# Kernel tuning notes

Measured on AMD Instinct MI355X. Metric: run time of the kernel, lower is better.

The kernel has to match this reference:

```python
import jax, jax.numpy as jnp
import numpy as np

B, T, E, D = 8, 2048, 1024, 64  # batch, seq_len, n_emb, head_dim

def setup_inputs() -> dict:
    key = jax.random.key(0)
    ks = jax.random.split(key, 4)
    scale = 1.0 / np.sqrt(E)
    return {
        "x": jax.random.normal(ks[0], (B, T, E), dtype=jnp.float32),
        "Wq": jax.random.normal(ks[1], (E, D), dtype=jnp.float32) * scale,
        "bq": jnp.zeros((D,), dtype=jnp.float32),
        "Wk": jax.random.normal(ks[2], (E, D), dtype=jnp.float32) * scale,
        "bk": jnp.zeros((D,), dtype=jnp.float32),
        "Wv": jax.random.normal(ks[3], (E, D), dtype=jnp.float32) * scale,
        "bv": jnp.zeros((D,), dtype=jnp.float32),
    }

def reference(x, Wq, bq, Wk, bk, Wv, bv):
    # QKV projections: [B,T,E] @ [E,D] -> [B,T,D]
    q = x @ Wq + bq
    k = x @ Wk + bk
    v = x @ Wv + bv
    d = q.shape[-1]
    # scaled dot-product scores [B,T,T]
    wei = jnp.einsum('btd,bsd->bts', q, k) * (d ** -0.5)
    # causal mask: position t attends to s <= t
    t = wei.shape[1]
    causal = jnp.tril(jnp.ones((t, t), dtype=bool))
    wei = jnp.where(causal, wei, -jnp.inf)
    wei = jax.nn.softmax(wei, axis=-1)
    # attention output [B,T,D]
    return jnp.einsum('bts,bsd->btd', wei, v)
```

## Files before the change

### kernel.cpp

```cpp
#include <hip/hip_runtime.h>
#include <math.h>


#define B_   8
#define T_   2048
#define E_   1024
#define D_   64
#define BT_  (B_ * T_)

typedef __attribute__((ext_vector_type(8))) short s16x8;
typedef __attribute__((ext_vector_type(4))) short s16x4;
typedef __attribute__((ext_vector_type(4))) float f32x4;

__device__ __forceinline__ short f2bf(float f) {
    union { float f; unsigned u; } a; a.f = f;
    unsigned r = a.u + 0x7fffu + ((a.u >> 16) & 1u);
    return (short)(r >> 16);
}

#define MFMA16(a, b, c) __builtin_amdgcn_mfma_f32_16x16x32_bf16((a), (b), (c), 0, 0, 0)

#define DPPF(x, ctrl) __builtin_bit_cast(float, \
    __builtin_amdgcn_update_dpp(0, __builtin_bit_cast(int, (x)), (ctrl), 0xF, 0xF, true))

__device__ __forceinline__ float rsum16(float x) {
    x += DPPF(x, 0xB1);
    x += DPPF(x, 0x4E);
    x += DPPF(x, 0x124);
    x += DPPF(x, 0x128);
    return x;
}

__global__ __launch_bounds__(256) void wtrans_kernel(
    const float* __restrict__ Wq, const float* __restrict__ Wk,
    const float* __restrict__ Wv, short* __restrict__ Wt)
{
    __shared__ float sT[64][65];
    const int sel = blockIdx.x >> 4;
    const int k0  = (blockIdx.x & 15) * 64;
    const float* W = sel == 0 ? Wq : (sel == 1 ? Wk : Wv);
    const int t  = threadIdx.x;
    const int kr = t >> 4, c4 = (t & 15) * 4;
    #pragma unroll
    for (int i = 0; i < 4; ++i) {
        float4 v = *(const float4*)&W[(size_t)(k0 + kr + i * 16) * D_ + c4];
        sT[kr + i * 16][c4 + 0] = v.x; sT[kr + i * 16][c4 + 1] = v.y;
        sT[kr + i * 16][c4 + 2] = v.z; sT[kr + i * 16][c4 + 3] = v.w;
    }
    __syncthreads();
    #pragma unroll
    for (int i = 0; i < 4; ++i) {
        int n  = (t >> 4) + i * 16;
        int kk = (t & 15) * 4;
        s16x4 o;
        o.x = f2bf(sT[kk + 0][n]); o.y = f2bf(sT[kk + 1][n]);
        o.z = f2bf(sT[kk + 2][n]); o.w = f2bf(sT[kk + 3][n]);
        *(s16x4*)&Wt[(size_t)(sel * 64 + n) * E_ + k0 + kk] = o;
    }
}

__global__ __launch_bounds__(256) void qkv_kernel(
    const float* __restrict__ x, const short* __restrict__ Wt,
    const float* __restrict__ bq, const float* __restrict__ bk,
    const float* __restrict__ bv,
    short* __restrict__ Qg, short* __restrict__ Kg, short* __restrict__ VTg)
{
    __shared__ short sX[2][32 * 76];
    const int tid  = threadIdx.x;
    const int lane = tid & 63;
    const int w    = tid >> 6;
    const int l15  = lane & 15, quad = lane >> 4;
    const int t0   = blockIdx.x * 32;
    const int bb   = t0 >> 11;

    const int srow = tid >> 3;
    const int skc  = (tid & 7) * 8;
    const float* px = &x[(size_t)(t0 + srow) * E_ + skc];

    f32x4 acc[3][2];
    #pragma unroll
    for (int a = 0; a < 3; ++a)
        #pragma unroll
        for (int h = 0; h < 2; ++h)
            acc[a][h] = (f32x4){0.f, 0.f, 0.f, 0.f};

    float4 ld0 = *(const float4*)px;
    float4 ld1 = *(const float4*)(px + 4);

    int buf = 0;
    for (int k0 = 0; k0 < E_; k0 += 64) {
        s16x8 pk;
        pk[0] = f2bf(ld0.x); pk[1] = f2bf(ld0.y); pk[2] = f2bf(ld0.z); pk[3] = f2bf(ld0.w);
        pk[4] = f2bf(ld1.x); pk[5] = f2bf(ld1.y); pk[6] = f2bf(ld1.z); pk[7] = f2bf(ld1.w);
        *(s16x8*)&sX[buf][srow * 76 + skc] = pk;
        __syncthreads();

        if (k0 + 64 < E_) {
            const float* p2 = px + k0 + 64;
            ld0 = *(const float4*)p2;
            ld1 = *(const float4*)(p2 + 4);
        }

        s16x8 aw[3][2];
        #pragma unroll
        for (int t3 = 0; t3 < 3; ++t3) {
            const short* pw = &Wt[(size_t)((w * 3 + t3) * 16 + l15) * E_ + k0 + quad * 8];
            aw[t3][0] = *(const s16x8*)pw;
            aw[t3][1] = *(const s16x8*)(pw + 32);
        }
        s16x8 bxf[2][2];
        #pragma unroll
        for (int h = 0; h < 2; ++h) {
            bxf[h][0] = *(const s16x8*)&sX[buf][(h * 16 + l15) * 76 + quad * 8];
            bxf[h][1] = *(const s16x8*)&sX[buf][(h * 16 + l15) * 76 + 32 + quad * 8];
        }
        #pragma unroll
        for (int t3 = 0; t3 < 3; ++t3)
            #pragma unroll
            for (int h = 0; h < 2; ++h) {
                acc[t3][h] = MFMA16(aw[t3][0], bxf[h][0], acc[t3][h]);
                acc[t3][h] = MFMA16(aw[t3][1], bxf[h][1], acc[t3][h]);
            }
        buf ^= 1;
    }

    __syncthreads();
    short* sVT = &sX[0][0];

    #pragma unroll
    for (int t3 = 0; t3 < 3; ++t3) {
        const int nt = w * 3 + t3;
        const int fb = (nt & 3) * 16 + quad * 4;
        const float* bias = nt < 4 ? bq : (nt < 8 ? bk : bv);
        f32x4 bsv = *(const f32x4*)&bias[fb];
        #pragma unroll
        for (int h = 0; h < 2; ++h) {
            const int tok = t0 + h * 16 + l15;
            f32x4 v = acc[t3][h] + bsv;
            if (nt < 4) {
                v *= 0.125f;
                s16x4 o = { f2bf(v[0]), f2bf(v[1]), f2bf(v[2]), f2bf(v[3]) };
                *(s16x4*)&Qg[(size_t)tok * D_ + fb] = o;
            } else if (nt < 8) {
                s16x4 o = { f2bf(v[0]), f2bf(v[1]), f2bf(v[2]), f2bf(v[3]) };
                *(s16x4*)&Kg[(size_t)tok * D_ + fb] = o;
            } else {
                const int lt = h * 16 + l15;
                #pragma unroll
                for (int r = 0; r < 4; ++r)
                    sVT[(fb + r) * 48 + lt] = f2bf(v[r]);
            }
        }
    }
    __syncthreads();
    {
        const int d  = tid >> 2;
        const int tq = (tid & 3) * 8;
        s16x8 vv = *(const s16x8*)&sVT[d * 48 + tq];
        *(s16x8*)&VTg[(size_t)(bb * D_ + d) * T_ + (t0 & (T_ - 1)) + tq] = vv;
    }
}

__global__ __launch_bounds__(256) void attn_kernel(
    const short* __restrict__ Qg, const short* __restrict__ Kg,
    const short* __restrict__ VTg, float* __restrict__ out)
{
    __shared__ char smem[20736];
    short* sP = (short*)smem;
    float* sO = (float*)smem;
    float* sl = (float*)(smem + 20480);

    const int tid  = threadIdx.x;
    const int lane = tid & 63;
    const int w    = tid >> 6;
    const int l15  = lane & 15, quad = lane >> 4;
    const int b    = blockIdx.x & 7;
    const int j    = 127 - (blockIdx.x >> 3);
    const int tq0  = j * 16;
    const int nch  = (j >> 2) + 1;
    const int seg  = (nch + 3) >> 2;
    const int c0   = w * seg;
    const int c1   = (c0 + seg < nch) ? c0 + seg : nch;

    const size_t qoff = ((size_t)b * T_ + tq0 + l15) * D_ + quad * 8;
    const s16x8 aq0 = *(const s16x8*)&Qg[qoff];
    const s16x8 aq1 = *(const s16x8*)&Qg[qoff + 32];

    f32x4 oacc[4];
    float lpart[4] = {0.f, 0.f, 0.f, 0.f};
    #pragma unroll
    for (int nt = 0; nt < 4; ++nt) oacc[nt] = (f32x4){0.f, 0.f, 0.f, 0.f};

    const short* kb = Kg  + (size_t)b * T_ * D_;
    const short* vb = VTg + (size_t)b * D_ * T_;
    short* sPw = sP + w * (16 * 72);

    for (int c = c0; c < c1; ++c) {
        const int s0 = c * 64;

        s16x8 bk[4][2];
        #pragma unroll
        for (int nt = 0; nt < 4; ++nt) {
            const short* pk = kb + (size_t)(s0 + nt * 16 + l15) * D_ + quad * 8;
            bk[nt][0] = *(const s16x8*)pk;
            bk[nt][1] = *(const s16x8*)(pk + 32);
        }
        const f32x4 zz = (f32x4){0.f, 0.f, 0.f, 0.f};
        f32x4 sacc[4];
        #pragma unroll
        for (int nt = 0; nt < 4; ++nt) {
            sacc[nt] = MFMA16(aq0, bk[nt][0], zz);
            sacc[nt] = MFMA16(aq1, bk[nt][1], sacc[nt]);
        }

        s16x8 bv[4][2];
        #pragma unroll
        for (int nt = 0; nt < 4; ++nt) {
            const short* pv = vb + (size_t)(nt * 16 + l15) * T_ + s0 + quad * 8;
            bv[nt][0] = *(const s16x8*)pv;
            bv[nt][1] = *(const s16x8*)(pv + 32);
        }

        const bool diag = (c == nch - 1);
        float p[4][4];
        #pragma unroll
        for (int nt = 0; nt < 4; ++nt)
            #pragma unroll
            for (int r = 0; r < 4; ++r) {
                float e = __expf(sacc[nt][r]);
                if (diag && (s0 + nt * 16 + l15 > tq0 + quad * 4 + r)) e = 0.f;
                p[nt][r] = e;
            }
        #pragma unroll
        for (int r = 0; r < 4; ++r)
            lpart[r] += (p[0][r] + p[1][r]) + (p[2][r] + p[3][r]);

        #pragma unroll
        for (int nt = 0; nt < 4; ++nt)
            #pragma unroll
            for (int r = 0; r < 4; ++r)
                sPw[(quad * 4 + r) * 72 + nt * 16 + l15] = f2bf(p[nt][r]);
        s16x8 ap0 = *(const s16x8*)&sPw[l15 * 72 + quad * 8];
        s16x8 ap1 = *(const s16x8*)&sPw[l15 * 72 + 32 + quad * 8];

        #pragma unroll
        for (int nt = 0; nt < 4; ++nt) {
            oacc[nt] = MFMA16(ap0, bv[nt][0], oacc[nt]);
            oacc[nt] = MFMA16(ap1, bv[nt][1], oacc[nt]);
        }
    }

    f32x4 lv;
    #pragma unroll
    for (int r = 0; r < 4; ++r) lv[r] = rsum16(lpart[r]);

    __syncthreads();
    float* sOw = sO + w * (64 * 20);
    #pragma unroll
    for (int nt = 0; nt < 4; ++nt)
        *(f32x4*)&sOw[(nt * 16 + l15) * 20 + quad * 4] = oacc[nt];
    if (l15 == 0)
        *(f32x4*)&sl[w * 16 + quad * 4] = lv;
    __syncthreads();

    const int d  = tid & 63;
    const int rb = (tid >> 6) * 4;
    f32x4 osum = (f32x4){0.f, 0.f, 0.f, 0.f};
    f32x4 lsum = (f32x4){0.f, 0.f, 0.f, 0.f};
    #pragma unroll
    for (int w2 = 0; w2 < 4; ++w2) {
        osum += *(const f32x4*)&sO[w2 * (64 * 20) + d * 20 + rb];
        lsum += *(const f32x4*)&sl[w2 * 16 + rb];
    }
    #pragma unroll
    for (int i = 0; i < 4; ++i)
        out[((size_t)b * T_ + tq0 + rb + i) * D_ + d] = osum[i] / lsum[i];
}

extern "C" void kernel_launch(void* const* d_in, const int* in_sizes, int n_in,
                              void* d_out, int out_size, void* d_ws, size_t ws_size,
                              hipStream_t stream) {
    (void)in_sizes; (void)n_in; (void)out_size; (void)ws_size;
    const float* x  = (const float*)d_in[0];
    const float* Wq = (const float*)d_in[1];
    const float* bq = (const float*)d_in[2];
    const float* Wk = (const float*)d_in[3];
    const float* bk = (const float*)d_in[4];
    const float* Wv = (const float*)d_in[5];
    const float* bv = (const float*)d_in[6];

    char* ws = (char*)d_ws;
    short* Qg  = (short*)(ws);
    short* Kg  = (short*)(ws + (size_t)2 * 1024 * 1024);
    short* VTg = (short*)(ws + (size_t)4 * 1024 * 1024);
    short* Wt  = (short*)(ws + (size_t)6 * 1024 * 1024);

    wtrans_kernel<<<48, 256, 0, stream>>>(Wq, Wk, Wv, Wt);
    qkv_kernel<<<BT_ / 32, 256, 0, stream>>>(x, Wt, bq, bk, bv, Qg, Kg, VTg);
    attn_kernel<<<B_ * 128, 256, 0, stream>>>(Qg, Kg, VTg, (float*)d_out);
}
```

Measured before the change: 167.8 us.

## Pair short and long causal query tiles per block; deepen x prefetch

The attention kernel now gives each block two 16-row query tiles, j and 127-j. Their combined key chunks are split evenly across the four waves, which balances the triangular causal work and halves the grid to 512 blocks. The QKV projection kernel also prefetches x two k-steps ahead instead of one, to hide more global-load latency. In exchange each attention block does two reductions through shared memory, needs more registers, and has fewer blocks to fill the GPU.

```diff
diff --git a/kernel.cpp b/kernel.cpp
--- a/kernel.cpp
+++ b/kernel.cpp
@@ -84,21 +84,26 @@
         for (int h = 0; h < 2; ++h)
             acc[a][h] = (f32x4){0.f, 0.f, 0.f, 0.f};
 
-    float4 ld0 = *(const float4*)px;
-    float4 ld1 = *(const float4*)(px + 4);
+    float4 lda0 = *(const float4*)px;
+    float4 lda1 = *(const float4*)(px + 4);
+    float4 ldb0 = *(const float4*)(px + 64);
+    float4 ldb1 = *(const float4*)(px + 68);
 
     int buf = 0;
     for (int k0 = 0; k0 < E_; k0 += 64) {
         s16x8 pk;
-        pk[0] = f2bf(ld0.x); pk[1] = f2bf(ld0.y); pk[2] = f2bf(ld0.z); pk[3] = f2bf(ld0.w);
-        pk[4] = f2bf(ld1.x); pk[5] = f2bf(ld1.y); pk[6] = f2bf(ld1.z); pk[7] = f2bf(ld1.w);
+        pk[0] = f2bf(lda0.x); pk[1] = f2bf(lda0.y);
+        pk[2] = f2bf(lda0.z); pk[3] = f2bf(lda0.w);
+        pk[4] = f2bf(lda1.x); pk[5] = f2bf(lda1.y);
+        pk[6] = f2bf(lda1.z); pk[7] = f2bf(lda1.w);
         *(s16x8*)&sX[buf][srow * 76 + skc] = pk;
         __syncthreads();
 
-        if (k0 + 64 < E_) {
-            const float* p2 = px + k0 + 64;
-            ld0 = *(const float4*)p2;
-            ld1 = *(const float4*)(p2 + 4);
+        lda0 = ldb0; lda1 = ldb1;
+        if (k0 + 128 < E_) {
+            const float* p2 = px + k0 + 128;
+            ldb0 = *(const float4*)p2;
+            ldb1 = *(const float4*)(p2 + 4);
         }
 
         s16x8 aw[3][2];
@@ -175,29 +180,37 @@
     const int w    = tid >> 6;
     const int l15  = lane & 15, quad = lane >> 4;
     const int b    = blockIdx.x & 7;
-    const int j    = 127 - (blockIdx.x >> 3);
-    const int tq0  = j * 16;
-    const int nch  = (j >> 2) + 1;
-    const int seg  = (nch + 3) >> 2;
+    const int pr   = blockIdx.x >> 3;
+    const int jA   = pr, jB = 127 - pr;
+    const int tqA  = jA * 16, tqB = jB * 16;
+    const int nchA = (jA >> 2) + 1, nchB = (jB >> 2) + 1;
+    const int tot  = nchA + nchB;
+    const int seg  = (tot + 3) >> 2;
     const int c0   = w * seg;
-    const int c1   = (c0 + seg < nch) ? c0 + seg : nch;
-
-    const size_t qoff = ((size_t)b * T_ + tq0 + l15) * D_ + quad * 8;
-    const s16x8 aq0 = *(const s16x8*)&Qg[qoff];
-    const s16x8 aq1 = *(const s16x8*)&Qg[qoff + 32];
-
-    f32x4 oacc[4];
-    float lpart[4] = {0.f, 0.f, 0.f, 0.f};
-    #pragma unroll
-    for (int nt = 0; nt < 4; ++nt) oacc[nt] = (f32x4){0.f, 0.f, 0.f, 0.f};
+    const int c1   = (c0 + seg < tot) ? c0 + seg : tot;
+
+    const size_t qoffA = ((size_t)b * T_ + tqA + l15) * D_ + quad * 8;
+    const s16x8 aqA0 = *(const s16x8*)&Qg[qoffA];
+    const s16x8 aqA1 = *(const s16x8*)&Qg[qoffA + 32];
+    const size_t qoffB = ((size_t)b * T_ + tqB + l15) * D_ + quad * 8;
+    const s16x8 aqB0 = *(const s16x8*)&Qg[qoffB];
+    const s16x8 aqB1 = *(const s16x8*)&Qg[qoffB + 32];
+
+    f32x4 oA[4], oB[4];
+    float lA[4] = {0.f, 0.f, 0.f, 0.f}, lB[4] = {0.f, 0.f, 0.f, 0.f};
+    #pragma unroll
+    for (int nt = 0; nt < 4; ++nt) {
+        oA[nt] = (f32x4){0.f, 0.f, 0.f, 0.f};
+        oB[nt] = (f32x4){0.f, 0.f, 0.f, 0.f};
+    }
 
     const short* kb = Kg  + (size_t)b * T_ * D_;
     const short* vb = VTg + (size_t)b * D_ * T_;
     short* sPw = sP + w * (16 * 72);
 
-    for (int c = c0; c < c1; ++c) {
-        const int s0 = c * 64;
-
+    auto body = [&](int cc, int tq, int nch, const s16x8& q0, const s16x8& q1,
+                    f32x4 (&oo)[4], float (&lp)[4]) {
+        const int s0 = cc * 64;
         s16x8 bk[4][2];
         #pragma unroll
         for (int nt = 0; nt < 4; ++nt) {
@@ -209,10 +222,9 @@
         f32x4 sacc[4];
         #pragma unroll
         for (int nt = 0; nt < 4; ++nt) {
-            sacc[nt] = MFMA16(aq0, bk[nt][0], zz);
-            sacc[nt] = MFMA16(aq1, bk[nt][1], sacc[nt]);
-        }
-
+            sacc[nt] = MFMA16(q0, bk[nt][0], zz);
+            sacc[nt] = MFMA16(q1, bk[nt][1], sacc[nt]);
+        }
         s16x8 bv[4][2];
         #pragma unroll
         for (int nt = 0; nt < 4; ++nt) {
@@ -220,21 +232,19 @@
             bv[nt][0] = *(const s16x8*)pv;
             bv[nt][1] = *(const s16x8*)(pv + 32);
         }
-
-        const bool diag = (c == nch - 1);
+        const bool diag = (cc == nch - 1);
         float p[4][4];
         #pragma unroll
         for (int nt = 0; nt < 4; ++nt)
             #pragma unroll
             for (int r = 0; r < 4; ++r) {
                 float e = __expf(sacc[nt][r]);
-                if (diag && (s0 + nt * 16 + l15 > tq0 + quad * 4 + r)) e = 0.f;
+                if (diag && (s0 + nt * 16 + l15 > tq + quad * 4 + r)) e = 0.f;
                 p[nt][r] = e;
             }
         #pragma unroll
         for (int r = 0; r < 4; ++r)
-            lpart[r] += (p[0][r] + p[1][r]) + (p[2][r] + p[3][r]);
-
+            lp[r] += (p[0][r] + p[1][r]) + (p[2][r] + p[3][r]);
         #pragma unroll
         for (int nt = 0; nt < 4; ++nt)
             #pragma unroll
@@ -242,39 +252,68 @@
                 sPw[(quad * 4 + r) * 72 + nt * 16 + l15] = f2bf(p[nt][r]);
         s16x8 ap0 = *(const s16x8*)&sPw[l15 * 72 + quad * 8];
         s16x8 ap1 = *(const s16x8*)&sPw[l15 * 72 + 32 + quad * 8];
-
         #pragma unroll
         for (int nt = 0; nt < 4; ++nt) {
-            oacc[nt] = MFMA16(ap0, bv[nt][0], oacc[nt]);
-            oacc[nt] = MFMA16(ap1, bv[nt][1], oacc[nt]);
-        }
-    }
-
-    f32x4 lv;
-    #pragma unroll
-    for (int r = 0; r < 4; ++r) lv[r] = rsum16(lpart[r]);
-
-    __syncthreads();
-    float* sOw = sO + w * (64 * 20);
-    #pragma unroll
-    for (int nt = 0; nt < 4; ++nt)
-        *(f32x4*)&sOw[(nt * 16 + l15) * 20 + quad * 4] = oacc[nt];
-    if (l15 == 0)
-        *(f32x4*)&sl[w * 16 + quad * 4] = lv;
-    __syncthreads();
+            oo[nt] = MFMA16(ap0, bv[nt][0], oo[nt]);
+            oo[nt] = MFMA16(ap1, bv[nt][1], oo[nt]);
+        }
+    };
+
+    for (int c = c0; c < c1; ++c) {
+        if (c < nchA) body(c, tqA, nchA, aqA0, aqA1, oA, lA);
+        else          body(c - nchA, tqB, nchB, aqB0, aqB1, oB, lB);
+    }
+
+    f32x4 lvA, lvB;
+    #pragma unroll
+    for (int r = 0; r < 4; ++r) { lvA[r] = rsum16(lA[r]); lvB[r] = rsum16(lB[r]); }
 
     const int d  = tid & 63;
     const int rb = (tid >> 6) * 4;
-    f32x4 osum = (f32x4){0.f, 0.f, 0.f, 0.f};
-    f32x4 lsum = (f32x4){0.f, 0.f, 0.f, 0.f};
-    #pragma unroll
-    for (int w2 = 0; w2 < 4; ++w2) {
-        osum += *(const f32x4*)&sO[w2 * (64 * 20) + d * 20 + rb];
-        lsum += *(const f32x4*)&sl[w2 * 16 + rb];
-    }
-    #pragma unroll
-    for (int i = 0; i < 4; ++i)
-        out[((size_t)b * T_ + tq0 + rb + i) * D_ + d] = osum[i] / lsum[i];
+
+    __syncthreads();
+    {
+        float* sOw = sO + w * (64 * 20);
+        #pragma unroll
+        for (int nt = 0; nt < 4; ++nt)
+            *(f32x4*)&sOw[(nt * 16 + l15) * 20 + quad * 4] = oA[nt];
+        if (l15 == 0) *(f32x4*)&sl[w * 16 + quad * 4] = lvA;
+    }
+    __syncthreads();
+    {
+        f32x4 osum = (f32x4){0.f, 0.f, 0.f, 0.f};
+        f32x4 lsum = (f32x4){0.f, 0.f, 0.f, 0.f};
+        #pragma unroll
+        for (int w2 = 0; w2 < 4; ++w2) {
+            osum += *(const f32x4*)&sO[w2 * (64 * 20) + d * 20 + rb];
+            lsum += *(const f32x4*)&sl[w2 * 16 + rb];
+        }
+        #pragma unroll
+        for (int i = 0; i < 4; ++i)
+            out[((size_t)b * T_ + tqA + rb + i) * D_ + d] = osum[i] / lsum[i];
+    }
+
+    __syncthreads();
+    {
+        float* sOw = sO + w * (64 * 20);
+        #pragma unroll
+        for (int nt = 0; nt < 4; ++nt)
+            *(f32x4*)&sOw[(nt * 16 + l15) * 20 + quad * 4] = oB[nt];
+        if (l15 == 0) *(f32x4*)&sl[w * 16 + quad * 4] = lvB;
+    }
+    __syncthreads();
+    {
+        f32x4 osum = (f32x4){0.f, 0.f, 0.f, 0.f};
+        f32x4 lsum = (f32x4){0.f, 0.f, 0.f, 0.f};
+        #pragma unroll
+        for (int w2 = 0; w2 < 4; ++w2) {
+            osum += *(const f32x4*)&sO[w2 * (64 * 20) + d * 20 + rb];
+            lsum += *(const f32x4*)&sl[w2 * 16 + rb];
+        }
+        #pragma unroll
+        for (int i = 0; i < 4; ++i)
+            out[((size_t)b * T_ + tqB + rb + i) * D_ + d] = osum[i] / lsum[i];
+    }
 }
 
 extern "C" void kernel_launch(void* const* d_in, const int* in_sizes, int n_in,
@@ -297,5 +336,5 @@
 
     wtrans_kernel<<<48, 256, 0, stream>>>(Wq, Wk, Wv, Wt);
     qkv_kernel<<<BT_ / 32, 256, 0, stream>>>(x, Wt, bq, bk, bv, Qg, Kg, VTg);
-    attn_kernel<<<B_ * 128, 256, 0, stream>>>(Qg, Kg, VTg, (float*)d_out);
-}
+    attn_kernel<<<B_ * 64, 256, 0, stream>>>(Qg, Kg, VTg, (float*)d_out);
+}
```

New measurement: 159.2 us. -5.1%, faster.
